# Performance work log

Hardware: AMD Instinct MI355X
Metric: run time of the kernel (lower is better)

## Reference

```python
import jax, jax.numpy as jnp
import numpy as np

B, S, D, H, P = 2, 2048, 1024, 16, 2048  # batch, q_len, d_model, heads, past_len
DEPTH = D // H
W_STD = 0.02


def setup_inputs() -> dict:
    key = jax.random.key(0)
    ks = jax.random.split(key, 5)
    x = jax.random.normal(ks[0], (B, S, D), dtype=jnp.float32)
    past_layer = jax.random.normal(ks[1], (B, 2, H, P, DEPTH), dtype=jnp.float32)
    w_attn = jax.random.normal(ks[2], (D, 3 * D), dtype=jnp.float32) * W_STD
    b_attn = jnp.zeros((3 * D,), dtype=jnp.float32)
    w_proj = jax.random.normal(ks[3], (D, D), dtype=jnp.float32) * W_STD
    b_proj = jnp.zeros((D,), dtype=jnp.float32)
    # causal mask with KV cache: query i sits at absolute position P+i; key j
    # is masked (1.0 -> +(-1e9)) when j > P + i.
    q_pos = P + jnp.arange(S)[:, None]        # [S,1]
    k_pos = jnp.arange(P + S)[None, :]        # [1,P+S]
    mask = (k_pos > q_pos).astype(jnp.float32)[None, None]  # [1,1,S,P+S]
    return {"x": x, "mask": mask, "past_layer": past_layer,
            "w_attn": w_attn, "b_attn": b_attn,
            "w_proj": w_proj, "b_proj": b_proj}


def _split_heads(t):
    # [B,S,D] -> [B,H,S,depth]
    b, s, _ = t.shape
    return t.reshape(b, s, H, DEPTH).transpose(0, 2, 1, 3)


def reference(x, mask, past_layer, w_attn, b_attn, w_proj, b_proj):
    # fused QKV projection (Conv1d == pointwise Linear)
    qkv = jnp.einsum('bsd,de->bse', x, w_attn) + b_attn        # [B,S,3D]
    q, k, v = jnp.split(qkv, 3, axis=2)
    q, k, v = _split_heads(q), _split_heads(k), _split_heads(v)
    # KV-cache concat
    k = jnp.concatenate([past_layer[:, 0], k], axis=2)         # [B,H,P+S,depth]
    v = jnp.concatenate([past_layer[:, 1], v], axis=2)
    present = jnp.stack([k, v], axis=1)                        # [B,2,H,P+S,depth]
    # scaled dot-product attention (full score matrix, eval mode: no dropout)
    scores = jnp.einsum('bhqd,bhkd->bhqk', q, k) / jnp.sqrt(
        jnp.asarray(DEPTH, dtype=jnp.float32))
    scores = scores + mask * (-1e9)
    attn = jax.nn.softmax(scores, axis=-1)
    ctx = jnp.einsum('bhqk,bhkd->bhqd', attn, v)               # [B,H,S,depth]
    merged = ctx.transpose(0, 2, 1, 3).reshape(B, S, D)
    output = jnp.einsum('bsd,de->bse', merged, w_proj) + b_proj
    return output, present
```

## Files before the change

kernel.cpp:

```cpp
#include <hip/hip_runtime.h>
#include <hip/hip_bf16.h>

#define B_ 2
#define S_ 2048
#define D_ 1024
#define H_ 16
#define P_ 2048
#define T_ 4096
#define DEPTH_ 64

typedef __bf16 bf16x8 __attribute__((ext_vector_type(8)));
typedef float  f32x4  __attribute__((ext_vector_type(4)));
typedef short  short8_t __attribute__((ext_vector_type(8)));
typedef unsigned short ushort_t;
typedef unsigned short ushort4_t __attribute__((ext_vector_type(4)));

__device__ __forceinline__ ushort_t f2bf(float f) {
    union { float f; unsigned u; } v; v.f = f;
    return (ushort_t)((v.u + 0x7fffu + ((v.u >> 16) & 1u)) >> 16);
}

__device__ __forceinline__ unsigned cvt_pk_bf16(float lo, float hi) {
    unsigned r;
    asm("v_cvt_pk_bf16_f32 %0, %1, %2" : "=v"(r) : "v"(lo), "v"(hi));
    return r;
}

__device__ __forceinline__ void gload16(const void* g, void* l) {
    __builtin_amdgcn_global_load_lds(
        (const __attribute__((address_space(1))) unsigned int*)g,
        (__attribute__((address_space(3))) unsigned int*)l, 16, 0, 0);
}

__global__ __launch_bounds__(256)
void convert_bf16_kernel(const float4* __restrict__ in, ushort4_t* __restrict__ out, int n4)
{
    for (int i = blockIdx.x * 256 + threadIdx.x; i < n4; i += gridDim.x * 256) {
        float4 v = in[i];
        ushort4_t o;
        o[0] = f2bf(v.x); o[1] = f2bf(v.y); o[2] = f2bf(v.z); o[3] = f2bf(v.w);
        out[i] = o;
    }
}

__global__ __launch_bounds__(256)
void transpose_conv_kernel(const float* __restrict__ w, ushort_t* __restrict__ wt, int N)
{
    __shared__ float t[64][65];
    const int tid = threadIdx.x;
    const int k0 = blockIdx.y * 64, n0 = blockIdx.x * 64;
    #pragma unroll
    for (int rep = 0; rep < 4; ++rep) {
        const int idx = rep * 256 + tid;
        const int r = idx >> 4, c = idx & 15;
        float4 v = *(const float4*)&w[(size_t)(k0 + r) * N + n0 + c * 4];
        t[r][c*4+0] = v.x; t[r][c*4+1] = v.y; t[r][c*4+2] = v.z; t[r][c*4+3] = v.w;
    }
    __syncthreads();
    #pragma unroll
    for (int rep = 0; rep < 4; ++rep) {
        const int idx = rep * 256 + tid;
        const int nl = idx >> 4, kg = idx & 15;
        ushort4_t o;
        o[0] = f2bf(t[kg*4+0][nl]); o[1] = f2bf(t[kg*4+1][nl]);
        o[2] = f2bf(t[kg*4+2][nl]); o[3] = f2bf(t[kg*4+3][nl]);
        *(ushort4_t*)&wt[(size_t)(n0 + nl) * 1024 + k0 + kg*4] = o;
    }
}

template<int MODE>
__global__ __launch_bounds__(256)
void gemm_bf16_kernel(const ushort_t* __restrict__ A,
                      const ushort_t* __restrict__ Bt,
                      const float*  __restrict__ bias,
                      ushort_t* __restrict__ out_qb,
                      float*  __restrict__ out_present,
                      float*  __restrict__ out_plain)
{
    __shared__ __attribute__((aligned(16))) ushort_t As[128*32];
    __shared__ __attribute__((aligned(16))) ushort_t Bs[128*32];

    const int tid  = threadIdx.x;
    const int w    = tid >> 6;
    const int lane = tid & 63;
    const int g    = lane >> 4;
    const int ln   = lane & 15;
    const int wr   = w >> 1, wc = w & 1;
    const int row0 = blockIdx.y * 128;
    const int col0 = blockIdx.x * 128;

    int srow[2], sgl[2];
    #pragma unroll
    for (int r = 0; r < 2; ++r) {
        const int o = (w*2 + r) * 1024 + lane * 16;
        srow[r] = o >> 6;
        const int gp = (o >> 4) & 3;
        sgl[r] = gp ^ ((srow[r] >> 1) & 3);
    }

    f32x4 acc[4][4];
    #pragma unroll
    for (int i = 0; i < 4; ++i)
        #pragma unroll
        for (int j = 0; j < 4; ++j)
            acc[i][j] = (f32x4){0.f, 0.f, 0.f, 0.f};

    for (int k0 = 0; k0 < 1024; k0 += 32) {
        #pragma unroll
        for (int r = 0; r < 2; ++r) {
            const int lb = (w*2 + r) * 512;
            gload16(&A [(size_t)(row0 + srow[r]) * 1024 + k0 + sgl[r]*8], &As[lb]);
            gload16(&Bt[(size_t)(col0 + srow[r]) * 1024 + k0 + sgl[r]*8], &Bs[lb]);
        }
        __syncthreads();

        bf16x8 af[4], bfr[4];
        #pragma unroll
        for (int i = 0; i < 4; ++i) {
            const int ra = wr*64 + i*16 + ln;
            const int ga = g ^ ((ra >> 1) & 3);
            af[i] = __builtin_bit_cast(bf16x8, *(const short8_t*)&As[ra*32 + ga*8]);
            const int rb = wc*64 + i*16 + ln;
            const int gb = g ^ ((rb >> 1) & 3);
            bfr[i] = __builtin_bit_cast(bf16x8, *(const short8_t*)&Bs[rb*32 + gb*8]);
        }
        #pragma unroll
        for (int i = 0; i < 4; ++i)
            #pragma unroll
            for (int j = 0; j < 4; ++j)
                acc[i][j] = __builtin_amdgcn_mfma_f32_16x16x32_bf16(af[i], bfr[j], acc[i][j], 0, 0, 0);
        __syncthreads();
    }

    #pragma unroll
    for (int i = 0; i < 4; ++i) {
        #pragma unroll
        for (int j = 0; j < 4; ++j) {
            const int rm = row0 + wr*64 + i*16 + g*4 + j;
            const int b  = rm >> 11;
            const int s  = rm & 2047;
            #pragma unroll
            for (int jn = 0; jn < 4; ++jn) {
                const int e = col0 + wc*64 + jn*16 + ln;
                const float v = acc[i][jn][j] + bias[e];
                if (MODE == 0) {
                    const int which = e >> 10;
                    const int f = e & 1023;
                    const int h = f >> 6, d = f & 63;
                    if (which == 0) {
                        out_qb[(size_t)(((b*16 + h) * 2048 + s) << 6) + d] =
                            f2bf(v * 0.18033688f);
                    } else {
                        const int kv = which - 1;
                        out_present[((((size_t)(b*2 + kv)*16 + h) * 4096 + 2048 + s) << 6) + d] = v;
                    }
                } else {
                    out_plain[(size_t)rm * 1024 + e] = v;
                }
            }
        }
    }
}

__global__ __launch_bounds__(256)
void prep_kv_kernel(const float* __restrict__ past,
                    float* __restrict__ present,
                    ushort_t* __restrict__ Kws, ushort_t* __restrict__ Vws)
{
    __shared__ float tv[64][65];
    const int tid = threadIdx.x;
    const int kt  = blockIdx.x;
    const int bh  = blockIdx.y;
    const int b   = bh >> 4, h = bh & 15;
    const bool old = (kt < 32);

    const float* Kp = old ? past    + (((size_t)(b*2+0)*16 + h) * P_ + kt*64) * 64
                          : present + (((size_t)(b*2+0)*16 + h) * T_ + kt*64) * 64;
    const float* Vp = old ? past    + (((size_t)(b*2+1)*16 + h) * P_ + kt*64) * 64
                          : present + (((size_t)(b*2+1)*16 + h) * T_ + kt*64) * 64;
    float4* PKo = (float4*)(present + (((size_t)(b*2+0)*16 + h) * T_ + kt*64) * 64);
    float4* PVo = (float4*)(present + (((size_t)(b*2+1)*16 + h) * T_ + kt*64) * 64);
    ushort_t* Kd = Kws + ((size_t)bh * T_ + kt*64) * 64;

    #pragma unroll
    for (int rep = 0; rep < 4; ++rep) {
        const int idx = rep * 256 + tid;
        float4 v = ((const float4*)Kp)[idx];
        if (old) PKo[idx] = v;
        ushort4_t o;
        o[0] = f2bf(v.x); o[1] = f2bf(v.y); o[2] = f2bf(v.z); o[3] = f2bf(v.w);
        *(ushort4_t*)&Kd[idx*4] = o;
        float4 vv = ((const float4*)Vp)[idx];
        if (old) PVo[idx] = vv;
        const int r = idx >> 4, c = idx & 15;
        tv[r][c*4+0] = vv.x; tv[r][c*4+1] = vv.y;
        tv[r][c*4+2] = vv.z; tv[r][c*4+3] = vv.w;
    }
    __syncthreads();
    #pragma unroll
    for (int rep = 0; rep < 4; ++rep) {
        const int idx = rep * 256 + tid;
        const int d = idx >> 4, pg = idx & 15;
        ushort4_t o;
        o[0] = f2bf(tv[pg*4+0][d]); o[1] = f2bf(tv[pg*4+1][d]);
        o[2] = f2bf(tv[pg*4+2][d]); o[3] = f2bf(tv[pg*4+3][d]);
        *(ushort4_t*)&Vws[((size_t)bh*64 + d) * T_ + kt*64 + pg*4] = o;
    }
}

__global__ __launch_bounds__(256, 2)
void attn_v14_kernel(const ushort_t* __restrict__ qin,
                     const ushort_t* __restrict__ Kws,
                     const ushort_t* __restrict__ Vws,
                     ushort_t* __restrict__ merged)
{
    __shared__ __attribute__((aligned(16))) ushort_t Kb[2][4096];
    __shared__ __attribute__((aligned(16))) ushort_t Vb[4][4096];
    __shared__ __attribute__((aligned(16))) ushort_t Pb[128*64];

    const int tid  = threadIdx.x;
    const int w    = tid >> 6;
    const int lane = tid & 63;
    const int g    = lane >> 4;
    const int ln   = lane & 15;
    const int lnm  = ln & 7;
    const int lsub = lane >> 3;
    const int swz8 = ((lane & 7) ^ lsub) * 8;

    const int bid = (int)blockIdx.x;
    const int a   = bid & 7;
    const int m_c = (bid >> 3) & 31;
    const int j   = bid >> 8;
    const int bh  = a * 4 + (m_c & 3);
    const int c   = m_c >> 2;
    const int qblk = (j == 0) ? c : (15 - c);
    const int q0   = qblk * 128;
    const int b    = bh >> 4, h = bh & 15;

    const ushort_t* Kbase = Kws + (size_t)bh * T_ * 64;
    const ushort_t* Vbase = Vws + (size_t)bh * 64 * T_;
    const int nt = 34 + 2 * qblk;

    const int kgOff0 = ((w*16 + 0 + lsub) << 6) + swz8;
    const int kgOff1 = ((w*16 + 8 + lsub) << 6) + swz8;
    const size_t vgOff0 = (size_t)(w*16 + 0 + lsub) * T_ + swz8;
    const size_t vgOff1 = (size_t)(w*16 + 8 + lsub) * T_ + swz8;
    const int ldsOff0 = (w*2 + 0) * 512;
    const int ldsOff1 = (w*2 + 1) * 512;
    const int pRow0 = (w*32 + ln) * 64;
    const int pRow1 = (w*32 + 16 + ln) * 64;

    gload16(Kbase + kgOff0, &Kb[0][ldsOff0]);
    gload16(Kbase + kgOff1, &Kb[0][ldsOff1]);
    gload16(Vbase + vgOff0, &Vb[0][ldsOff0]);
    gload16(Vbase + vgOff1, &Vb[0][ldsOff1]);
    gload16(Vbase + vgOff0 + 64, &Vb[1][ldsOff0]);
    gload16(Vbase + vgOff1 + 64, &Vb[1][ldsOff1]);

    bf16x8 qf[2][2];
    #pragma unroll
    for (int qg = 0; qg < 2; ++qg) {
        const ushort_t* Qr = qin + ((size_t)bh * S_ + q0 + w*32 + qg*16 + ln) * 64;
        #pragma unroll
        for (int kh = 0; kh < 2; ++kh)
            qf[qg][kh] = __builtin_bit_cast(bf16x8, *(const short8_t*)(Qr + kh*32 + g*8));
    }

    f32x4 o[2][4];
    #pragma unroll
    for (int qg = 0; qg < 2; ++qg)
        #pragma unroll
        for (int d = 0; d < 4; ++d) o[qg][d] = (f32x4){0.f, 0.f, 0.f, 0.f};
    float l0 = 0.f, l1 = 0.f;

    auto pv_step = [&](const ushort_t* vbase) {
        __builtin_amdgcn_s_setprio(1);
        #pragma unroll
        for (int kh = 0; kh < 2; ++kh) {
            bf16x8 pf0 = __builtin_bit_cast(bf16x8,
                           *(const short8_t*)&Pb[pRow0 + (((kh*4 + g) ^ lnm) << 3)]);
            bf16x8 pf1 = __builtin_bit_cast(bf16x8,
                           *(const short8_t*)&Pb[pRow1 + (((kh*4 + g) ^ lnm) << 3)]);
            #pragma unroll
            for (int dsub = 0; dsub < 4; ++dsub) {
                const ushort_t* vr = vbase + (dsub*16 + ln) * 64;
                bf16x8 va = __builtin_bit_cast(bf16x8,
                              *(const short8_t*)(vr + ((kh*4 + g) ^ lnm)*8));
                o[0][dsub] = __builtin_amdgcn_mfma_f32_16x16x32_bf16(va, pf0, o[0][dsub], 0, 0, 0);
                o[1][dsub] = __builtin_amdgcn_mfma_f32_16x16x32_bf16(va, pf1, o[1][dsub], 0, 0, 0);
            }
        }
        __builtin_amdgcn_s_setprio(0);
    };

#define ATTN_STEP(KCUR, KNXT, VPRV, VISS)                                       \
    {                                                                           \
        if (t + 1 < nt) { asm volatile("s_waitcnt vmcnt(2)" ::: "memory"); }    \
        else            { asm volatile("s_waitcnt vmcnt(0)" ::: "memory"); }    \
        __builtin_amdgcn_s_barrier();                                           \
        __builtin_amdgcn_sched_barrier(0);                                      \
        if (t + 1 < nt) {                                                       \
            const size_t t0n = (size_t)(t + 1) * 64;                            \
            gload16(Kbase + (t0n << 6) + kgOff0, &Kb[KNXT][ldsOff0]);           \
            gload16(Kbase + (t0n << 6) + kgOff1, &Kb[KNXT][ldsOff1]);           \
        }                                                                       \
        if (t + 2 < nt) {                                                       \
            const size_t t0v = (size_t)(t + 2) * 64;                            \
            gload16(Vbase + vgOff0 + t0v, &Vb[VISS][ldsOff0]);                  \
            gload16(Vbase + vgOff1 + t0v, &Vb[VISS][ldsOff1]);                  \
        }                                                                       \
        __builtin_amdgcn_sched_barrier(0);                                      \
        f32x4 st[2][4];                                                         \
        __builtin_amdgcn_s_setprio(1);                                          \
        _Pragma("unroll")                                                       \
        for (int js = 0; js < 4; ++js) {                                        \
            const ushort_t* kr = &Kb[KCUR][(js*16 + ln) * 64];                  \
            bf16x8 a0 = __builtin_bit_cast(bf16x8, *(const short8_t*)(kr + ((    g) ^ lnm)*8)); \
            bf16x8 a1 = __builtin_bit_cast(bf16x8, *(const short8_t*)(kr + ((4 + g) ^ lnm)*8)); \
            _Pragma("unroll")                                                   \
            for (int qg = 0; qg < 2; ++qg) {                                    \
                f32x4 z = (f32x4){0.f, 0.f, 0.f, 0.f};                          \
                z = __builtin_amdgcn_mfma_f32_16x16x32_bf16(a0, qf[qg][0], z, 0, 0, 0); \
                z = __builtin_amdgcn_mfma_f32_16x16x32_bf16(a1, qf[qg][1], z, 0, 0, 0); \
                st[qg][js] = z;                                                 \
            }                                                                   \
        }                                                                       \
        __builtin_amdgcn_s_setprio(0);                                          \
                                             \
        if (t > 0) pv_step(&Vb[VPRV][0]);                                       \
        if (t >= nt - 2) {                                                      \
            const int off = t*64 - 2048 - q0;                                   \
            _Pragma("unroll")                                                   \
            for (int qg = 0; qg < 2; ++qg) {                                    \
                const int wrow = w*32 + qg*16 + ln;                             \
                _Pragma("unroll")                                               \
                for (int js = 0; js < 4; ++js)                                  \
                    _Pragma("unroll")                                           \
                    for (int r = 0; r < 4; ++r)                                 \
                        if (js*16 + g*4 + r + off > wrow) st[qg][js][r] = -1e30f; \
            }                                                                   \
        }                                                                       \
                \
        _Pragma("unroll")                                                       \
        for (int qg = 0; qg < 2; ++qg) {                                        \
            const int pR = qg ? pRow1 : pRow0;                                  \
            float rs = 0.f;                                                     \
            _Pragma("unroll")                                                   \
            for (int js = 0; js < 4; ++js) {                                    \
                float p0 = exp2f(st[qg][js][0]);                                \
                float p1 = exp2f(st[qg][js][1]);                                \
                float p2 = exp2f(st[qg][js][2]);                                \
                float p3 = exp2f(st[qg][js][3]);                                \
                rs += (p0 + p1) + (p2 + p3);                                    \
                uint2 pk;                                                       \
                pk.x = cvt_pk_bf16(p0, p1);                                     \
                pk.y = cvt_pk_bf16(p2, p3);                                     \
                *(uint2*)&Pb[pR + (((js*4 + g) ^ (lnm << 1)) << 2)] = pk;       \
            }                                                                   \
            if (qg) l1 += rs; else l0 += rs;                                    \
        }                                                                       \
    }

    int t = 0;
    for (;;) {
        ATTN_STEP(0, 1, 3, 2);
        if (++t == nt) break;
        ATTN_STEP(1, 0, 0, 3);
        if (++t == nt) break;
        ATTN_STEP(0, 1, 1, 0);
        if (++t == nt) break;
        ATTN_STEP(1, 0, 2, 1);
        if (++t == nt) break;
    }
#undef ATTN_STEP

    pv_step(&Vb[(nt - 1) & 3][0]);

    float lf0 = l0 + __shfl_xor(l0, 16); lf0 += __shfl_xor(lf0, 32);
    float lf1 = l1 + __shfl_xor(l1, 16); lf1 += __shfl_xor(lf1, 32);
    #pragma unroll
    for (int qg = 0; qg < 2; ++qg) {
        const float inv = 1.f / (qg ? lf1 : lf0);
        const int row = q0 + w*32 + qg*16 + ln;
        #pragma unroll
        for (int dsub = 0; dsub < 4; ++dsub) {
            ushort4_t ov;
            ov[0] = f2bf(o[qg][dsub][0] * inv);
            ov[1] = f2bf(o[qg][dsub][1] * inv);
            ov[2] = f2bf(o[qg][dsub][2] * inv);
            ov[3] = f2bf(o[qg][dsub][3] * inv);
            *(ushort4_t*)&merged[((size_t)b * S_ + row) * D_ + h*64 + dsub*16 + g*4] = ov;
        }
    }
}

extern "C" void kernel_launch(void* const* d_in, const int* in_sizes, int n_in,
                              void* d_out, int out_size, void* d_ws, size_t ws_size,
                              hipStream_t stream)
{
    const float* x      = (const float*)d_in[0];
    const float* past   = (const float*)d_in[2];
    const float* w_attn = (const float*)d_in[3];
    const float* b_attn = (const float*)d_in[4];
    const float* w_proj = (const float*)d_in[5];
    const float* b_proj = (const float*)d_in[6];

    float* out     = (float*)d_out;
    float* present = out + (size_t)B_ * S_ * D_;

    ushort_t* wsu     = (ushort_t*)d_ws;
    ushort_t* q_ws    = wsu;
    ushort_t* mergedb = wsu + 4194304;
    ushort_t* wptb    = wsu + 8388608;
    ushort_t* xb      = wsu + 9437184;
    ushort_t* watb    = wsu + 13631488;
    ushort_t* K_ws    = wsu + 9437184;
    ushort_t* V_ws    = wsu + 17825792;

    convert_bf16_kernel<<<2048, 256, 0, stream>>>(
        (const float4*)x, (ushort4_t*)xb, (B_*S_*D_)/4);
    transpose_conv_kernel<<<dim3(48, 16), 256, 0, stream>>>(w_attn, watb, 3072);
    transpose_conv_kernel<<<dim3(16, 16), 256, 0, stream>>>(w_proj, wptb, 1024);

    gemm_bf16_kernel<0><<<dim3(24, 32), 256, 0, stream>>>(
        xb, watb, b_attn, q_ws, present, nullptr);

    prep_kv_kernel<<<dim3(64, 32), 256, 0, stream>>>(past, present, K_ws, V_ws);

    attn_v14_kernel<<<dim3(512), 256, 0, stream>>>(q_ws, K_ws, V_ws, mergedb);

    gemm_bf16_kernel<1><<<dim3(8, 32), 256, 0, stream>>>(
        mergedb, wptb, b_proj, nullptr, nullptr, out);
}
```

Before: 186.1 us.

## Fuse new K/V bf16 workspace writes into QKV GEMM epilogue and merge transposes

The QKV GEMM epilogue now writes the bf16 K and V attention workspaces directly for the new tokens, with V stored transposed via packed 4-element stores. This lets the prep kernel handle only the past-cache half, so new K/V are no longer re-read from present. The two weight transpose kernels are merged into one launch using blockIdx.z. K/V workspace offsets move so they no longer alias xb, because the GEMM writes them while still reading xb. The epilogue loop is reordered so each column's four rows are handled together.

```diff
diff --git a/kernel.cpp b/kernel.cpp
--- a/kernel.cpp
+++ b/kernel.cpp
@@ -44,8 +44,15 @@
 }
 
 __global__ __launch_bounds__(256)
-void transpose_conv_kernel(const float* __restrict__ w, ushort_t* __restrict__ wt, int N)
-{
+void transpose_conv2_kernel(const float* __restrict__ wa, ushort_t* __restrict__ wta,
+                            const float* __restrict__ wp, ushort_t* __restrict__ wtp)
+{
+    const int z = blockIdx.z;
+    if (z == 1 && blockIdx.x >= 16) return;
+    const float* w = z ? wp : wa;
+    ushort_t* wt = z ? wtp : wta;
+    const int N = z ? 1024 : 3072;
+
     __shared__ float t[64][65];
     const int tid = threadIdx.x;
     const int k0 = blockIdx.y * 64, n0 = blockIdx.x * 64;
@@ -75,6 +82,8 @@
                       const float*  __restrict__ bias,
                       ushort_t* __restrict__ out_qb,
                       float*  __restrict__ out_present,
+                      ushort_t* __restrict__ out_kws,
+                      ushort_t* __restrict__ out_vws,
                       float*  __restrict__ out_plain)
 {
     __shared__ __attribute__((aligned(16))) ushort_t As[128*32];
@@ -134,50 +143,62 @@
 
     #pragma unroll
     for (int i = 0; i < 4; ++i) {
-        #pragma unroll
-        for (int j = 0; j < 4; ++j) {
-            const int rm = row0 + wr*64 + i*16 + g*4 + j;
-            const int b  = rm >> 11;
-            const int s  = rm & 2047;
+        const int rm0 = row0 + wr*64 + i*16 + g*4;
+        const int b   = rm0 >> 11;
+        const int s0  = rm0 & 2047;
+        #pragma unroll
+        for (int jn = 0; jn < 4; ++jn) {
+            const int e = col0 + wc*64 + jn*16 + ln;
+            float vv[4];
             #pragma unroll
-            for (int jn = 0; jn < 4; ++jn) {
-                const int e = col0 + wc*64 + jn*16 + ln;
-                const float v = acc[i][jn][j] + bias[e];
-                if (MODE == 0) {
-                    const int which = e >> 10;
-                    const int f = e & 1023;
-                    const int h = f >> 6, d = f & 63;
-                    if (which == 0) {
-                        out_qb[(size_t)(((b*16 + h) * 2048 + s) << 6) + d] =
-                            f2bf(v * 0.18033688f);
-                    } else {
-                        const int kv = which - 1;
-                        out_present[((((size_t)(b*2 + kv)*16 + h) * 4096 + 2048 + s) << 6) + d] = v;
+            for (int j = 0; j < 4; ++j) vv[j] = acc[i][jn][j] + bias[e];
+            if (MODE == 0) {
+                const int which = e >> 10;
+                const int f = e & 1023;
+                const int h = f >> 6, d = f & 63;
+                const int bh = b*16 + h;
+                if (which == 0) {
+                    #pragma unroll
+                    for (int j = 0; j < 4; ++j)
+                        out_qb[(size_t)(((bh) * 2048 + s0 + j) << 6) + d] =
+                            f2bf(vv[j] * 0.18033688f);
+                } else if (which == 1) {
+                    #pragma unroll
+                    for (int j = 0; j < 4; ++j) {
+                        out_present[((((size_t)(b*2)*16 + h) * 4096 + 2048 + s0 + j) << 6) + d] = vv[j];
+                        out_kws[(((size_t)bh * T_ + 2048 + s0 + j) << 6) + d] = f2bf(vv[j]);
                     }
                 } else {
-                    out_plain[(size_t)rm * 1024 + e] = v;
+                    ushort4_t pk;
+                    #pragma unroll
+                    for (int j = 0; j < 4; ++j) {
+                        out_present[((((size_t)(b*2 + 1)*16 + h) * 4096 + 2048 + s0 + j) << 6) + d] = vv[j];
+                        pk[j] = f2bf(vv[j]);
+                    }
+                    *(ushort4_t*)&out_vws[((size_t)bh*64 + d) * T_ + 2048 + s0] = pk;
                 }
+            } else {
+                #pragma unroll
+                for (int j = 0; j < 4; ++j)
+                    out_plain[(size_t)(rm0 + j) * 1024 + e] = vv[j];
             }
         }
     }
 }
 
 __global__ __launch_bounds__(256)
-void prep_kv_kernel(const float* __restrict__ past,
-                    float* __restrict__ present,
-                    ushort_t* __restrict__ Kws, ushort_t* __restrict__ Vws)
+void prep_kv_old_kernel(const float* __restrict__ past,
+                        float* __restrict__ present,
+                        ushort_t* __restrict__ Kws, ushort_t* __restrict__ Vws)
 {
     __shared__ float tv[64][65];
     const int tid = threadIdx.x;
     const int kt  = blockIdx.x;
     const int bh  = blockIdx.y;
     const int b   = bh >> 4, h = bh & 15;
-    const bool old = (kt < 32);
-
-    const float* Kp = old ? past    + (((size_t)(b*2+0)*16 + h) * P_ + kt*64) * 64
-                          : present + (((size_t)(b*2+0)*16 + h) * T_ + kt*64) * 64;
-    const float* Vp = old ? past    + (((size_t)(b*2+1)*16 + h) * P_ + kt*64) * 64
-                          : present + (((size_t)(b*2+1)*16 + h) * T_ + kt*64) * 64;
+
+    const float* Kp = past + (((size_t)(b*2+0)*16 + h) * P_ + kt*64) * 64;
+    const float* Vp = past + (((size_t)(b*2+1)*16 + h) * P_ + kt*64) * 64;
     float4* PKo = (float4*)(present + (((size_t)(b*2+0)*16 + h) * T_ + kt*64) * 64);
     float4* PVo = (float4*)(present + (((size_t)(b*2+1)*16 + h) * T_ + kt*64) * 64);
     ushort_t* Kd = Kws + ((size_t)bh * T_ + kt*64) * 64;
@@ -186,12 +207,12 @@
     for (int rep = 0; rep < 4; ++rep) {
         const int idx = rep * 256 + tid;
         float4 v = ((const float4*)Kp)[idx];
-        if (old) PKo[idx] = v;
+        PKo[idx] = v;
         ushort4_t o;
         o[0] = f2bf(v.x); o[1] = f2bf(v.y); o[2] = f2bf(v.z); o[3] = f2bf(v.w);
         *(ushort4_t*)&Kd[idx*4] = o;
         float4 vv = ((const float4*)Vp)[idx];
-        if (old) PVo[idx] = vv;
+        PVo[idx] = vv;
         const int r = idx >> 4, c = idx & 15;
         tv[r][c*4+0] = vv.x; tv[r][c*4+1] = vv.y;
         tv[r][c*4+2] = vv.z; tv[r][c*4+3] = vv.w;
@@ -326,7 +347,6 @@
             }                                                                   \
         }                                                                       \
         __builtin_amdgcn_s_setprio(0);                                          \
-                                             \
         if (t > 0) pv_step(&Vb[VPRV][0]);                                       \
         if (t >= nt - 2) {                                                      \
             const int off = t*64 - 2048 - q0;                                   \
@@ -340,7 +360,6 @@
                         if (js*16 + g*4 + r + off > wrow) st[qg][js][r] = -1e30f; \
             }                                                                   \
         }                                                                       \
-                \
         _Pragma("unroll")                                                       \
         for (int qg = 0; qg < 2; ++qg) {                                        \
             const int pR = qg ? pRow1 : pRow0;                                  \
@@ -414,21 +433,21 @@
     ushort_t* wptb    = wsu + 8388608;
     ushort_t* xb      = wsu + 9437184;
     ushort_t* watb    = wsu + 13631488;
-    ushort_t* K_ws    = wsu + 9437184;
-    ushort_t* V_ws    = wsu + 17825792;
+    ushort_t* K_ws    = wsu + 16777216;
+    ushort_t* V_ws    = wsu + 25165824;
 
     convert_bf16_kernel<<<2048, 256, 0, stream>>>(
         (const float4*)x, (ushort4_t*)xb, (B_*S_*D_)/4);
-    transpose_conv_kernel<<<dim3(48, 16), 256, 0, stream>>>(w_attn, watb, 3072);
-    transpose_conv_kernel<<<dim3(16, 16), 256, 0, stream>>>(w_proj, wptb, 1024);
+    transpose_conv2_kernel<<<dim3(48, 16, 2), 256, 0, stream>>>(
+        w_attn, watb, w_proj, wptb);
 
     gemm_bf16_kernel<0><<<dim3(24, 32), 256, 0, stream>>>(
-        xb, watb, b_attn, q_ws, present, nullptr);
-
-    prep_kv_kernel<<<dim3(64, 32), 256, 0, stream>>>(past, present, K_ws, V_ws);
+        xb, watb, b_attn, q_ws, present, K_ws, V_ws, nullptr);
+
+    prep_kv_old_kernel<<<dim3(32, 32), 256, 0, stream>>>(past, present, K_ws, V_ws);
 
     attn_v14_kernel<<<dim3(512), 256, 0, stream>>>(q_ws, K_ws, V_ws, mergedb);
 
     gemm_bf16_kernel<1><<<dim3(8, 32), 256, 0, stream>>>(
-        mergedb, wptb, b_proj, nullptr, nullptr, out);
-}
+        mergedb, wptb, b_proj, nullptr, nullptr, nullptr, nullptr, out);
+}
```

After: 184.5 us. About the same (-0.8%).
